# Kernel tuning notes

Measured on AMD Instinct MI355X. Metric: run time of the kernel, lower is better.

The kernel has to match this reference:

```python
import jax, jax.numpy as jnp
import numpy as np
from jax import lax

W_SCALE = 0.1   # brevitas SignedBinaryWeightPerTensorConst default scaling_init
A_SCALE = 1.0   # SignedBinaryActPerTensorConst: min/max = -1/1 -> scale 1
BN_EPS = 1e-5


def _bin_w(w):
    # sign(w) * const scale, straight-through estimator (identity STE as in brevitas binary_sign_ste)
    q = jnp.where(w >= 0, W_SCALE, -W_SCALE).astype(w.dtype)
    return w + lax.stop_gradient(q - w)


def _bin_act(x):
    # QuantHardTanh with binary act quant: output is sign(x)*1, STE passes grad inside [-1,1]
    c = jnp.clip(x, -A_SCALE, A_SCALE)
    q = jnp.where(x >= 0, A_SCALE, -A_SCALE).astype(x.dtype)
    return c + lax.stop_gradient(q - c)


def _conv(x, w, b, stride=(1, 1), pad=((0, 0), (0, 0))):
    y = lax.conv_general_dilated(x, _bin_w(w), window_strides=stride, padding=pad,
                                 dimension_numbers=('NCHW', 'OIHW', 'NCHW'))
    return y + b[None, :, None, None]


def _bn(x, gamma, beta):
    # training-mode BatchNorm2d: batch statistics over (N, H, W)
    mu = jnp.mean(x, axis=(0, 2, 3), keepdims=True)
    var = jnp.var(x, axis=(0, 2, 3), keepdims=True)
    inv = lax.rsqrt(var + BN_EPS)
    return (x - mu) * inv * gamma[None, :, None, None] + beta[None, :, None, None]


def _pool2x1(x):
    # MaxPool2d((2,1)) with floor: drop trailing odd row
    N, C, H, W = x.shape
    h2 = H // 2
    return x[:, :, : 2 * h2].reshape(N, C, h2, 2, W).max(axis=3)


def setup_inputs() -> dict:
    key = jax.random.key(0)
    ks = jax.random.split(key, 10)
    nC = 128
    d = {
        'x':  jax.random.normal(ks[0], (64, 1, 16000, 1), jnp.float32),
        'w1': jax.random.normal(ks[1], (nC, 1, 84, 1), jnp.float32) * 0.05,
        'b1': jnp.zeros((nC,), jnp.float32),
        'g1': jnp.ones((nC,), jnp.float32), 'be1': jnp.zeros((nC,), jnp.float32),
        'w2': jax.random.normal(ks[2], (nC, nC, 4, 1), jnp.float32) * 0.05,
        'b2': jnp.zeros((nC,), jnp.float32),
        'g2': jnp.ones((nC,), jnp.float32), 'be2': jnp.zeros((nC,), jnp.float32),
        'w3': jax.random.normal(ks[3], (2 * nC, nC, 4, 1), jnp.float32) * 0.05,
        'b3': jnp.zeros((2 * nC,), jnp.float32),
        'g3': jnp.ones((2 * nC,), jnp.float32), 'be3': jnp.zeros((2 * nC,), jnp.float32),
        'w5': jax.random.normal(ks[4], (4 * nC, 2 * nC, 3, 1), jnp.float32) * 0.05,
        'b5': jnp.zeros((4 * nC,), jnp.float32),
        'g5': jnp.ones((4 * nC,), jnp.float32), 'be5': jnp.zeros((4 * nC,), jnp.float32),
        'wfc': jax.random.normal(ks[5], (35, 4 * nC * 249), jnp.float32) * 0.01,
    }
    return d


def reference(x, w1, b1, g1, be1, w2, b2, g2, be2, w3, b3, g3, be3,
              w5, b5, g5, be5, wfc):
    h = _conv(x, w1, b1, stride=(4, 1))                     # [B,128,3980,1]
    h = _pool2x1(_bin_act(_bn(h, g1, be1)))                 # [B,128,1990,1]
    h = _conv(h, w2, b2, pad=((2, 2), (0, 0)))              # [B,128,1991,1]
    h = _pool2x1(_bin_act(_bn(h, g2, be2)))                 # [B,128,995,1]
    h = _conv(h, w3, b3, pad=((1, 1), (0, 0)))              # [B,256,994,1]
    h = _pool2x1(_bin_act(_bn(h, g3, be3)))                 # [B,256,497,1]
    h = _conv(h, w5, b5, pad=((2, 2), (0, 0)))              # [B,512,499,1]
    h = _pool2x1(_bin_act(_bn(h, g5, be5)))                 # [B,512,249,1]
    h = h.reshape(h.shape[0], -1)                           # [B, 512*249]
    return h @ _bin_w(wfc).T                                # [B, 35]
```

## Files before the change

### kernel.cpp

```cpp
#include <hip/hip_runtime.h>
#include <stdint.h>


constexpr int Bn  = 64;
constexpr int H1  = 3980;
constexpr int J1  = 1990;
constexpr int H2o = 1991, J2 = 995;
constexpr int H3o = 994,  J3 = 497;
constexpr int H5o = 499,  J5 = 249;
constexpr int FCW = 249 * 8;

__global__ void binarize_all(const float* __restrict__ w2, const float* __restrict__ w3,
                             const float* __restrict__ w5, const float* __restrict__ wfc,
                             const float* __restrict__ w1,
                             uint64_t* __restrict__ wb2, uint64_t* __restrict__ wb3,
                             uint64_t* __restrict__ wb5, uint64_t* __restrict__ wbf,
                             float* __restrict__ w1pk)
{
    int idx = blockIdx.x * 256 + threadIdx.x;
    if (idx < 1024) {
        int wdx = idx & 1, k = (idx >> 1) & 3, c = idx >> 3;
        uint64_t v = 0;
        for (int ci = 0; ci < 64; ++ci)
            if (w2[((size_t)c * 128 + (wdx * 64 + ci)) * 4 + k] >= 0.f) v |= 1ull << ci;
        wb2[idx] = v;
    } else if (idx < 3072) {
        int t = idx - 1024;
        int wdx = t & 1, k = (t >> 1) & 3, c = t >> 3;
        uint64_t v = 0;
        for (int ci = 0; ci < 64; ++ci)
            if (w3[((size_t)c * 128 + (wdx * 64 + ci)) * 4 + k] >= 0.f) v |= 1ull << ci;
        wb3[t] = v;
    } else if (idx < 9216) {
        int t = idx - 3072;
        int wdx = t & 3, k = (t >> 2) % 3, c = t / 12;
        uint64_t v = 0;
        for (int ci = 0; ci < 64; ++ci)
            if (w5[((size_t)c * 256 + (wdx * 64 + ci)) * 3 + k] >= 0.f) v |= 1ull << ci;
        wb5[t] = v;
    } else if (idx < 9216 + 69720) {
        int t = idx - 9216;
        int wdx = t & 7, hh = (t >> 3) % 249, oc = t / (249 * 8);
        uint64_t v = 0;
        for (int ci = 0; ci < 64; ++ci)
            if (wfc[(size_t)oc * 127488 + (size_t)(wdx * 64 + ci) * 249 + hh] >= 0.f)
                v |= 1ull << ci;
        wbf[t] = v;
    } else if (idx < 9216 + 69720 + 10752) {
        int t  = idx - (9216 + 69720);
        int G  = t / 672, r = t % 672;
        int kg = r >> 5;
        int e  = r & 31;
        int u  = e >> 2, jj = e & 3;
        w1pk[t] = (w1[(size_t)(G * 8 + u) * 84 + kg * 4 + jj] >= 0.f) ? 0.1f : -0.1f;
    }
}

#define ROW_FMA(A, XV) \
    A[u] = fmaf(wv.x, XV.x, A[u]); A[u] = fmaf(wv.y, XV.y, A[u]); \
    A[u] = fmaf(wv.z, XV.z, A[u]); A[u] = fmaf(wv.w, XV.w, A[u]);
#define ROW_STAT(A, HOFF) { \
    const int h = h0 + (HOFF) + tid; \
    if (h < H1) { const float v = A[u] + bv; base[h] = v; \
                  s += (double)v; q += (double)v * v; } }

__global__ __launch_bounds__(256) void conv1_y1(
    const float* __restrict__ x, const float4* __restrict__ w1pk,
    const float* __restrict__ b1, float* __restrict__ y1,
    double2* __restrict__ part)
{
    __shared__ float4 xs4[2068];
    __shared__ float4 wl[336];
    __shared__ double2 statw[4][16];
    const int n   = blockIdx.y;
    const int bh  = blockIdx.x;
    const int h0  = bh << 11;
    const int z   = blockIdx.z;
    const int tid = threadIdx.x;
    const int wave = tid >> 6, lane = tid & 63;

    const float4* x4 = (const float4*)x + (size_t)n * 4000;
    for (int i = tid; i < 2068; i += 256) {
        const int gi = h0 + i;
        xs4[i] = (gi < 4000) ? x4[gi] : make_float4(0.f, 0.f, 0.f, 0.f);
    }
    const float4* wsrc = w1pk + (size_t)z * 336;
    for (int i = tid; i < 336; i += 256) wl[i] = wsrc[i];
    __syncthreads();

    for (int g = 0; g < 2; ++g) {
        float a0[8] = {0,0,0,0,0,0,0,0};
        float a1r[8] = {0,0,0,0,0,0,0,0};
        float a2[8] = {0,0,0,0,0,0,0,0};
        float a3[8] = {0,0,0,0,0,0,0,0};
        float a4[8] = {0,0,0,0,0,0,0,0};
        float a5[8] = {0,0,0,0,0,0,0,0};
        float a6[8] = {0,0,0,0,0,0,0,0};
        float a7[8] = {0,0,0,0,0,0,0,0};
        #pragma unroll 3
        for (int kg = 0; kg < 21; ++kg) {
            const float4 xv0 = xs4[tid + kg];
            const float4 xv1 = xs4[tid + 256 + kg];
            const float4 xv2 = xs4[tid + 512 + kg];
            const float4 xv3 = xs4[tid + 768 + kg];
            const float4 xv4 = xs4[tid + 1024 + kg];
            const float4 xv5 = xs4[tid + 1280 + kg];
            const float4 xv6 = xs4[tid + 1536 + kg];
            const float4 xv7 = xs4[tid + 1792 + kg];
            const float4* wk = &wl[(g * 21 + kg) * 8];
            #pragma unroll
            for (int u = 0; u < 8; ++u) {
                const float4 wv = wk[u];
                ROW_FMA(a0, xv0)
                ROW_FMA(a1r, xv1)
                ROW_FMA(a2, xv2)
                ROW_FMA(a3, xv3)
                ROW_FMA(a4, xv4)
                ROW_FMA(a5, xv5)
                ROW_FMA(a6, xv6)
                ROW_FMA(a7, xv7)
            }
        }
        #pragma unroll
        for (int u = 0; u < 8; ++u) {
            const int c = z * 16 + g * 8 + u;
            const float bv = b1[c];
            float* base = y1 + ((size_t)n * 128 + c) * H1;
            double s = 0.0, q = 0.0;
            ROW_STAT(a0, 0)
            ROW_STAT(a1r, 256)
            ROW_STAT(a2, 512)
            ROW_STAT(a3, 768)
            ROW_STAT(a4, 1024)
            ROW_STAT(a5, 1280)
            ROW_STAT(a6, 1536)
            ROW_STAT(a7, 1792)
            #pragma unroll
            for (int o = 32; o > 0; o >>= 1) {
                s += __shfl_xor(s, o, 64);
                q += __shfl_xor(q, o, 64);
            }
            if (lane == 0) statw[wave][g * 8 + u] = make_double2(s, q);
        }
    }
    __syncthreads();
    if (tid < 16) {
        const double2 p0 = statw[0][tid], p1v = statw[1][tid];
        const double2 p2 = statw[2][tid], p3  = statw[3][tid];
        part[((size_t)((n * 2 + bh) * 8 + z)) * 16 + tid] =
            make_double2(((p0.x + p1v.x) + p2.x) + p3.x,
                         ((p0.y + p1v.y) + p2.y) + p3.y);
    }
}

__global__ __launch_bounds__(128) void bn_reduce1(const double2* __restrict__ part,
                                                  float2* __restrict__ bnp)
{
    __shared__ double sS[128], sQ[128];
    const int c = blockIdx.x, t = threadIdx.x;
    const int z = c >> 4, cl = c & 15;
    const double2 p = part[((size_t)(t * 8 + z)) * 16 + cl];
    sS[t] = p.x; sQ[t] = p.y;
    __syncthreads();
    for (int o = 64; o > 0; o >>= 1) {
        if (t < o) { sS[t] += sS[t + o]; sQ[t] += sQ[t + o]; }
        __syncthreads();
    }
    if (t == 0) {
        const double N = (double)Bn * H1;
        const double mu  = sS[0] / N;
        const double var = sQ[0] / N - mu * mu;
        bnp[c] = make_float2((float)mu, (float)(1.0 / sqrt(var + 1e-5)));
    }
}

__global__ __launch_bounds__(256) void signpool1_y(
    const float* __restrict__ y1, const float2* __restrict__ bnp,
    const float* __restrict__ g1, const float* __restrict__ be1,
    uint64_t* __restrict__ a1)
{
    __shared__ float2 smi[128];
    __shared__ float  sg[128], sbe[128];
    const int n   = blockIdx.y;
    const int tid = threadIdx.x;
    const int j2  = blockIdx.x * 256 + tid;
    if (tid < 128) { smi[tid] = bnp[tid]; sg[tid] = g1[tid]; sbe[tid] = be1[tid]; }
    __syncthreads();
    if (j2 >= 995) return;
    uint64_t w0a = 0, w1a = 0, w0b = 0, w1b = 0;
    for (int c = 0; c < 128; ++c) {
        const float4 v = *(const float4*)(y1 + ((size_t)n * 128 + c) * H1 + 4 * j2);
        const float2 mi = smi[c];
        const float gg = sg[c], bb = sbe[c];
        const float t0 = __fadd_rn(__fmul_rn(__fmul_rn(__fsub_rn(v.x, mi.x), mi.y), gg), bb);
        const float t1 = __fadd_rn(__fmul_rn(__fmul_rn(__fsub_rn(v.y, mi.x), mi.y), gg), bb);
        const float t2 = __fadd_rn(__fmul_rn(__fmul_rn(__fsub_rn(v.z, mi.x), mi.y), gg), bb);
        const float t3 = __fadd_rn(__fmul_rn(__fmul_rn(__fsub_rn(v.w, mi.x), mi.y), gg), bb);
        const uint64_t ba = ((t0 >= 0.f) || (t1 >= 0.f)) ? 1ull : 0ull;
        const uint64_t bbit = ((t2 >= 0.f) || (t3 >= 0.f)) ? 1ull : 0ull;
        if (c < 64) { w0a |= ba << c;        w0b |= bbit << c; }
        else        { w1a |= ba << (c - 64); w1b |= bbit << (c - 64); }
    }
    uint64_t* dst = a1 + ((size_t)n * J1 + 2 * j2) * 2;
    dst[0] = w0a; dst[1] = w1a; dst[2] = w0b; dst[3] = w1b;
}

template<int CINW, int KK, int PAD, int COUT>
__global__ __launch_bounds__(COUT) void bconv_stats(
    const uint64_t* __restrict__ ain, const uint64_t* __restrict__ wb,
    const int HIN, const int HOUT, int* __restrict__ part)
{
    __shared__ uint64_t rows[(64 + KK - 1) * CINW];
    const int n  = blockIdx.y;
    const int h0 = blockIdx.x << 6;
    const int c  = threadIdx.x;
    for (int i = c; i < (64 + KK - 1) * CINW; i += COUT) {
        int r = h0 - PAD + i / CINW;
        rows[i] = (r >= 0 && r < HIN) ? ain[((size_t)n * HIN + r) * CINW + (i % CINW)] : 0ull;
    }
    __syncthreads();
    uint64_t wreg[KK * CINW];
    #pragma unroll
    for (int i = 0; i < KK * CINW; ++i) wreg[i] = wb[(size_t)c * KK * CINW + i];
    int pcw[KK];
    #pragma unroll
    for (int k = 0; k < KK; ++k) {
        int pc = 0;
        #pragma unroll
        for (int wd = 0; wd < CINW; ++wd) pc += __popcll(wreg[k * CINW + wd]);
        pcw[k] = pc;
    }
    int sq = 0, sq2 = 0;
    const int hmax = min(64, HOUT - h0);
    for (int i = 0; i < hmax; ++i) {
        const int h = h0 + i;
        int X = 0;
        #pragma unroll
        for (int k = 0; k < KK; ++k)
            #pragma unroll
            for (int wd = 0; wd < CINW; ++wd)
                X += __popcll(rows[(i + k) * CINW + wd] ^ wreg[k * CINW + wd]);
        int q = 64 * CINW * KK - 2 * X;
        if (h < PAD || h > HIN + PAD - KK) {
            #pragma unroll
            for (int k = 0; k < KK; ++k)
                if (k < PAD - h || k >= HIN + PAD - h)
                    q -= 64 * CINW - 2 * pcw[k];
        }
        sq += q; sq2 += q * q;
    }
    const size_t blk = (size_t)n * gridDim.x + blockIdx.x;
    part[(blk * COUT + c) * 2 + 0] = sq;
    part[(blk * COUT + c) * 2 + 1] = sq2;
}

template<int CINW, int KK, int PAD, int COUT>
__global__ __launch_bounds__(COUT) void bconv_sign(
    const uint64_t* __restrict__ ain, const uint64_t* __restrict__ wb,
    const int HIN, const int HOUT, const int J,
    const float* __restrict__ bias, const float2* __restrict__ bnp,
    const float* __restrict__ g, const float* __restrict__ be,
    uint64_t* __restrict__ aout)
{
    constexpr int W = COUT / 64;
    __shared__ uint64_t rows[(64 + KK - 1) * CINW];
    const int n  = blockIdx.y;
    const int h0 = blockIdx.x << 6;
    const int c  = threadIdx.x;
    for (int i = c; i < (64 + KK - 1) * CINW; i += COUT) {
        int r = h0 - PAD + i / CINW;
        rows[i] = (r >= 0 && r < HIN) ? ain[((size_t)n * HIN + r) * CINW + (i % CINW)] : 0ull;
    }
    __syncthreads();
    uint64_t wreg[KK * CINW];
    #pragma unroll
    for (int i = 0; i < KK * CINW; ++i) wreg[i] = wb[(size_t)c * KK * CINW + i];
    int pcw[KK];
    #pragma unroll
    for (int k = 0; k < KK; ++k) {
        int pc = 0;
        #pragma unroll
        for (int wd = 0; wd < CINW; ++wd) pc += __popcll(wreg[k * CINW + wd]);
        pcw[k] = pc;
    }
    const float bb = bias[c], gg = g[c], bbe = be[c];
    const float2 mi = bnp[c];
    const int wv = c >> 6, lane = c & 63;
    uint64_t prev = 0;
    const int hmax = min(64, HOUT - h0);
    for (int i = 0; i < hmax; ++i) {
        const int h = h0 + i;
        int X = 0;
        #pragma unroll
        for (int k = 0; k < KK; ++k)
            #pragma unroll
            for (int wd = 0; wd < CINW; ++wd)
                X += __popcll(rows[(i + k) * CINW + wd] ^ wreg[k * CINW + wd]);
        int q = 64 * CINW * KK - 2 * X;
        if (h < PAD || h > HIN + PAD - KK) {
            #pragma unroll
            for (int k = 0; k < KK; ++k)
                if (k < PAD - h || k >= HIN + PAD - h)
                    q -= 64 * CINW - 2 * pcw[k];
        }
        const float y = __fadd_rn(__fmul_rn(0.1f, (float)q), bb);
        const float t = __fadd_rn(__fmul_rn(__fmul_rn(__fsub_rn(y, mi.x), mi.y), gg), bbe);
        const uint64_t word = __ballot(t >= 0.f);
        if (i & 1) {
            const int j = h >> 1;
            if (lane == 0 && j < J)
                aout[((size_t)n * J + j) * W + wv] = prev | word;
        } else {
            prev = word;
        }
    }
}

__global__ __launch_bounds__(256) void bn_reduce_q(
    const int* __restrict__ part, const int nblk, const int C,
    const double N, const float* __restrict__ bias, float2* __restrict__ bnp)
{
    __shared__ long long sS[256], sQ[256];
    const int c = blockIdx.x, t = threadIdx.x;
    long long Sq = 0, Sq2 = 0;
    for (int b = t; b < nblk; b += 256) {
        const int2 p = *(const int2*)(part + ((size_t)b * C + c) * 2);
        Sq += p.x; Sq2 += p.y;
    }
    sS[t] = Sq; sQ[t] = Sq2;
    __syncthreads();
    for (int o = 128; o > 0; o >>= 1) {
        if (t < o) { sS[t] += sS[t + o]; sQ[t] += sQ[t + o]; }
        __syncthreads();
    }
    if (t == 0) {
        const double bb = (double)bias[c];
        const double S  = 0.1 * (double)sS[0] + N * bb;
        const double SS = 0.01 * (double)sQ[0] + 0.2 * bb * (double)sS[0] + N * bb * bb;
        const double mu = S / N;
        const double var = SS / N - mu * mu;
        bnp[c] = make_float2((float)mu, (float)(1.0 / sqrt(var + 1e-5)));
    }
}

__global__ void fc_kernel(const uint64_t* __restrict__ a5, const uint64_t* __restrict__ wfcb,
                          float* __restrict__ out)
{
    const int n    = blockIdx.y;
    const int oc   = blockIdx.x * 4 + (threadIdx.x >> 6);
    const int lane = threadIdx.x & 63;
    if (oc >= 35) return;
    const uint64_t* arow = a5   + (size_t)n  * FCW;
    const uint64_t* wrow = wfcb + (size_t)oc * FCW;
    int X = 0;
    for (int i = lane; i < FCW; i += 64)
        X += __popcll(arow[i] ^ wrow[i]);
    for (int o = 32; o > 0; o >>= 1) X += __shfl_xor(X, o, 64);
    if (lane == 0) out[(size_t)n * 35 + oc] = 0.1f * (float)(127488 - 2 * X);
}

extern "C" void kernel_launch(void* const* d_in, const int* in_sizes, int n_in,
                              void* d_out, int out_size, void* d_ws, size_t ws_size,
                              hipStream_t stream)
{
    (void)in_sizes; (void)n_in; (void)out_size;
    const float* x   = (const float*)d_in[0];
    const float* w1  = (const float*)d_in[1];
    const float* b1  = (const float*)d_in[2];
    const float* g1  = (const float*)d_in[3];
    const float* be1 = (const float*)d_in[4];
    const float* w2  = (const float*)d_in[5];
    const float* b2  = (const float*)d_in[6];
    const float* g2  = (const float*)d_in[7];
    const float* be2 = (const float*)d_in[8];
    const float* w3  = (const float*)d_in[9];
    const float* b3  = (const float*)d_in[10];
    const float* g3  = (const float*)d_in[11];
    const float* be3 = (const float*)d_in[12];
    const float* w5  = (const float*)d_in[13];
    const float* b5  = (const float*)d_in[14];
    const float* g5  = (const float*)d_in[15];
    const float* be5 = (const float*)d_in[16];
    const float* wfc = (const float*)d_in[17];
    char* ws = (char*)d_ws;

    size_t cur = 0;
    auto take = [&](size_t bytes) {
        size_t r = cur;
        cur = (cur + bytes + 255) & ~(size_t)255;
        return r;
    };
    const size_t off_y1 = take(130416640);
    float*    y1  = (float*)(ws + off_y1);
    int*      pq  = (int*)(ws + off_y1 + 35651584);
    uint64_t* a1  = (uint64_t*)(ws + take(2037760));
    uint64_t* a2  = (uint64_t*)(ws + take(1018880));
    uint64_t* a3  = (uint64_t*)(ws + take(1017856));
    uint64_t* a5  = (uint64_t*)(ws + take(1019904));
    uint64_t* wb2 = (uint64_t*)(ws + take(8192));
    uint64_t* wb3 = (uint64_t*)(ws + take(16384));
    uint64_t* wb5 = (uint64_t*)(ws + take(49152));
    uint64_t* wbf = (uint64_t*)(ws + take(557760));
    float*    w1pk = (float*)(ws + take(43008));
    double2*  p1  = (double2*)(ws + take(262144));
    float2*   bnp1 = (float2*)(ws + take(1024));
    float2*   bnp2 = (float2*)(ws + take(1024));
    float2*   bnp3 = (float2*)(ws + take(2048));
    float2*   bnp5 = (float2*)(ws + take(4096));
    if (cur > ws_size) return;

    hipLaunchKernelGGL(binarize_all, dim3(351), dim3(256), 0, stream,
                       w2, w3, w5, wfc, w1, wb2, wb3, wb5, wbf, w1pk);
    hipLaunchKernelGGL(conv1_y1, dim3(2, 64, 8), dim3(256), 0, stream,
                       x, (const float4*)w1pk, b1, y1, p1);
    hipLaunchKernelGGL(bn_reduce1, dim3(128), dim3(128), 0, stream, p1, bnp1);
    hipLaunchKernelGGL(signpool1_y, dim3(4, 64), dim3(256), 0, stream,
                       y1, bnp1, g1, be1, a1);
    hipLaunchKernelGGL((bconv_stats<2, 4, 2, 128>), dim3(32, 64), dim3(128), 0, stream,
                       a1, wb2, J1, H2o, pq);
    hipLaunchKernelGGL(bn_reduce_q, dim3(128), dim3(256), 0, stream,
                       pq, 2048, 128, (double)Bn * H2o, b2, bnp2);
    hipLaunchKernelGGL((bconv_sign<2, 4, 2, 128>), dim3(32, 64), dim3(128), 0, stream,
                       a1, wb2, J1, H2o, J2, b2, bnp2, g2, be2, a2);
    hipLaunchKernelGGL((bconv_stats<2, 4, 1, 256>), dim3(16, 64), dim3(256), 0, stream,
                       a2, wb3, J2, H3o, pq);
    hipLaunchKernelGGL(bn_reduce_q, dim3(256), dim3(256), 0, stream,
                       pq, 1024, 256, (double)Bn * H3o, b3, bnp3);
    hipLaunchKernelGGL((bconv_sign<2, 4, 1, 256>), dim3(16, 64), dim3(256), 0, stream,
                       a2, wb3, J2, H3o, J3, b3, bnp3, g3, be3, a3);
    hipLaunchKernelGGL((bconv_stats<4, 3, 2, 512>), dim3(8, 64), dim3(512), 0, stream,
                       a3, wb5, J3, H5o, pq);
    hipLaunchKernelGGL(bn_reduce_q, dim3(512), dim3(256), 0, stream,
                       pq, 512, 512, (double)Bn * H5o, b5, bnp5);
    hipLaunchKernelGGL((bconv_sign<4, 3, 2, 512>), dim3(8, 64), dim3(512), 0, stream,
                       a3, wb5, J3, H5o, J5, b5, bnp5, g5, be5, a5);
    hipLaunchKernelGGL(fc_kernel, dim3(9, 64), dim3(256), 0, stream,
                       a5, wbf, (float*)d_out);
}
```

Measured before the change: 338.7 us.

## Split FC weight binarization into ballot kernel and halve signpool channel loop

FC weight binarization moves out of the monolithic binarize_all into its own kernel. There, each wavefront's lanes read 64 input channels and build each 64-bit mask with __ballot instead of a serial 64-iteration loop per thread. signpool1_y now splits the 128 channels across two thread halves, each writing one 64-bit word, doubling the grid so more threads run and each does less serial work. This adds a kernel launch, and the FC kernel uses only 280 small blocks with strided reads.

```diff
diff --git a/kernel.cpp b/kernel.cpp
--- a/kernel.cpp
+++ b/kernel.cpp
@@ -11,11 +11,9 @@
 constexpr int FCW = 249 * 8;
 
 __global__ void binarize_all(const float* __restrict__ w2, const float* __restrict__ w3,
-                             const float* __restrict__ w5, const float* __restrict__ wfc,
-                             const float* __restrict__ w1,
+                             const float* __restrict__ w5, const float* __restrict__ w1,
                              uint64_t* __restrict__ wb2, uint64_t* __restrict__ wb3,
-                             uint64_t* __restrict__ wb5, uint64_t* __restrict__ wbf,
-                             float* __restrict__ w1pk)
+                             uint64_t* __restrict__ wb5, float* __restrict__ w1pk)
 {
     int idx = blockIdx.x * 256 + threadIdx.x;
     if (idx < 1024) {
@@ -38,21 +36,25 @@
         for (int ci = 0; ci < 64; ++ci)
             if (w5[((size_t)c * 256 + (wdx * 64 + ci)) * 3 + k] >= 0.f) v |= 1ull << ci;
         wb5[t] = v;
-    } else if (idx < 9216 + 69720) {
-        int t = idx - 9216;
-        int wdx = t & 7, hh = (t >> 3) % 249, oc = t / (249 * 8);
-        uint64_t v = 0;
-        for (int ci = 0; ci < 64; ++ci)
-            if (wfc[(size_t)oc * 127488 + (size_t)(wdx * 64 + ci) * 249 + hh] >= 0.f)
-                v |= 1ull << ci;
-        wbf[t] = v;
-    } else if (idx < 9216 + 69720 + 10752) {
-        int t  = idx - (9216 + 69720);
+    } else if (idx < 9216 + 10752) {
+        int t  = idx - 9216;
         int G  = t / 672, r = t % 672;
         int kg = r >> 5;
         int e  = r & 31;
         int u  = e >> 2, jj = e & 3;
         w1pk[t] = (w1[(size_t)(G * 8 + u) * 84 + kg * 4 + jj] >= 0.f) ? 0.1f : -0.1f;
+    }
+}
+
+__global__ __launch_bounds__(64) void binarize_fc(const float* __restrict__ wfc,
+                                                  uint64_t* __restrict__ wbf)
+{
+    const int oc = blockIdx.x, wdx = blockIdx.y, lane = threadIdx.x;
+    const float* src = wfc + (size_t)oc * 127488 + (size_t)(wdx * 64 + lane) * 249;
+    uint64_t* dst = wbf + (size_t)oc * FCW + wdx;
+    for (int hh = 0; hh < 249; ++hh) {
+        const uint64_t b = __ballot(src[hh] >= 0.f);
+        if (lane == 0) dst[(size_t)hh * 8] = b;
     }
 }
 
@@ -183,12 +185,14 @@
     __shared__ float  sg[128], sbe[128];
     const int n   = blockIdx.y;
     const int tid = threadIdx.x;
-    const int j2  = blockIdx.x * 256 + tid;
     if (tid < 128) { smi[tid] = bnp[tid]; sg[tid] = g1[tid]; sbe[tid] = be1[tid]; }
     __syncthreads();
+    const int j2   = blockIdx.x * 128 + (tid & 127);
+    const int half = tid >> 7;
     if (j2 >= 995) return;
-    uint64_t w0a = 0, w1a = 0, w0b = 0, w1b = 0;
-    for (int c = 0; c < 128; ++c) {
+    uint64_t wa = 0, wb = 0;
+    for (int i = 0; i < 64; ++i) {
+        const int c = half * 64 + i;
         const float4 v = *(const float4*)(y1 + ((size_t)n * 128 + c) * H1 + 4 * j2);
         const float2 mi = smi[c];
         const float gg = sg[c], bb = sbe[c];
@@ -196,13 +200,12 @@
         const float t1 = __fadd_rn(__fmul_rn(__fmul_rn(__fsub_rn(v.y, mi.x), mi.y), gg), bb);
         const float t2 = __fadd_rn(__fmul_rn(__fmul_rn(__fsub_rn(v.z, mi.x), mi.y), gg), bb);
         const float t3 = __fadd_rn(__fmul_rn(__fmul_rn(__fsub_rn(v.w, mi.x), mi.y), gg), bb);
-        const uint64_t ba = ((t0 >= 0.f) || (t1 >= 0.f)) ? 1ull : 0ull;
-        const uint64_t bbit = ((t2 >= 0.f) || (t3 >= 0.f)) ? 1ull : 0ull;
-        if (c < 64) { w0a |= ba << c;        w0b |= bbit << c; }
-        else        { w1a |= ba << (c - 64); w1b |= bbit << (c - 64); }
-    }
-    uint64_t* dst = a1 + ((size_t)n * J1 + 2 * j2) * 2;
-    dst[0] = w0a; dst[1] = w1a; dst[2] = w0b; dst[3] = w1b;
+        if ((t0 >= 0.f) || (t1 >= 0.f)) wa |= 1ull << i;
+        if ((t2 >= 0.f) || (t3 >= 0.f)) wb |= 1ull << i;
+    }
+    uint64_t* dst = a1 + ((size_t)n * J1 + 2 * j2) * 2 + half;
+    dst[0] = wa;
+    dst[2] = wb;
 }
 
 template<int CINW, int KK, int PAD, int COUT>
@@ -409,12 +412,13 @@
     float2*   bnp5 = (float2*)(ws + take(4096));
     if (cur > ws_size) return;
 
-    hipLaunchKernelGGL(binarize_all, dim3(351), dim3(256), 0, stream,
-                       w2, w3, w5, wfc, w1, wb2, wb3, wb5, wbf, w1pk);
+    hipLaunchKernelGGL(binarize_all, dim3(78), dim3(256), 0, stream,
+                       w2, w3, w5, w1, wb2, wb3, wb5, w1pk);
+    hipLaunchKernelGGL(binarize_fc, dim3(35, 8), dim3(64), 0, stream, wfc, wbf);
     hipLaunchKernelGGL(conv1_y1, dim3(2, 64, 8), dim3(256), 0, stream,
                        x, (const float4*)w1pk, b1, y1, p1);
     hipLaunchKernelGGL(bn_reduce1, dim3(128), dim3(128), 0, stream, p1, bnp1);
-    hipLaunchKernelGGL(signpool1_y, dim3(4, 64), dim3(256), 0, stream,
+    hipLaunchKernelGGL(signpool1_y, dim3(8, 64), dim3(256), 0, stream,
                        y1, bnp1, g1, be1, a1);
     hipLaunchKernelGGL((bconv_stats<2, 4, 2, 128>), dim3(32, 64), dim3(128), 0, stream,
                        a1, wb2, J1, H2o, pq);
```

Result: slower. 382.6 us (+13.0%).
